# Kernel tuning notes

Hardware: AMD Instinct MI355X
Metric: run time of the kernel (lower is better)

## Reference

```python
import jax, jax.numpy as jnp
import numpy as np

BLOCK_M = 64          # Triton BLOCK_M assumed from first autotune config
SPEAKER, SCENE, STAGE = 1, 2, 3
NUM_HEADS, HEAD_SIZE = 12, 64


def setup_inputs() -> dict:
    key = jax.random.key(0)
    ks = jax.random.split(key, 6)
    B, T, E = 4, 1024, 768
    H, D = NUM_HEADS, HEAD_SIZE
    x = jax.random.normal(ks[0], (B, T, E), jnp.float32)
    idx = jax.random.randint(ks[1], (B, T), 0, 32000)
    struct_embed = jax.random.normal(ks[2], (4, E), jnp.float32) * 0.02
    w_qkv = jax.random.normal(ks[3], (3 * H * D, E), jnp.float32) * 0.02
    w_out = jax.random.normal(ks[4], (E, H * D), jnp.float32) * 0.02
    b_out = jnp.zeros((E,), jnp.float32)
    return {"x": x, "idx": idx, "struct_embed": struct_embed,
            "w_qkv": w_qkv, "w_out": w_out, "b_out": b_out}


def _attention(q, k, v):
    # q,k,v: [B,H,T,D]. Faithful to the Triton kernel (eval mode):
    # q/k rounded to bf16, fp32 dot, logit clamp [-30,30], exp clamp 1e5,
    # +1e-10 denom, output rounded to bf16. Query rows with
    # (row % BLOCK_M) % 3 == 0 are zeroed by the kernel's load mask.
    T, D = q.shape[2], q.shape[3]
    keep = ((jnp.arange(T) % BLOCK_M) % 3 != 0).astype(q.dtype)
    qb = q.astype(jnp.bfloat16).astype(jnp.float32) * keep[None, None, :, None]
    kb = k.astype(jnp.bfloat16).astype(jnp.float32)
    scale = 1.0 / np.sqrt(D).astype(np.float32)
    scores = jnp.einsum('bhmd,bhnd->bhmn', qb, kb) * scale
    scores = jnp.clip(scores, -30.0, 30.0)
    m = jnp.max(scores, axis=-1, keepdims=True)
    p = jnp.minimum(jnp.exp(scores - m), 1e5)
    acc = jnp.einsum('bhmn,bhnd->bhmd', p, v)
    out = acc / (jnp.sum(p, axis=-1, keepdims=True) + 1e-10)
    return out.astype(jnp.bfloat16).astype(jnp.float32)


def reference(x, idx, struct_embed, w_qkv, w_out, b_out):
    B, T, E = x.shape
    H, D = NUM_HEADS, HEAD_SIZE
    # structure embedding addition (struct_dropout is identity in eval)
    struct_ids = ((idx == SPEAKER) * 1 + (idx == SCENE) * 2
                  + (idx == STAGE) * 3)
    x = x + struct_embed[struct_ids]
    # fused QKV projection (no bias)
    qkv = x @ w_qkv.T                              # [B,T,3HD]
    q, k, v = jnp.split(qkv, 3, axis=-1)
    q = q.reshape(B, T, H, D).transpose(0, 2, 1, 3)
    k = k.reshape(B, T, H, D).transpose(0, 2, 1, 3)
    v = v.reshape(B, T, H, D).transpose(0, 2, 1, 3)
    attn = _attention(q, k, v)                     # [B,H,T,D]
    attn = attn.transpose(0, 2, 1, 3).reshape(B, T, H * D)
    return attn @ w_out.T + b_out
```

## Files before the change

### kernel.cpp

```cpp
#include <hip/hip_runtime.h>
#include <hip/hip_bf16.h>

typedef __attribute__((ext_vector_type(8))) short bf16x8;
typedef __attribute__((ext_vector_type(4))) short bf16x4;
typedef __attribute__((ext_vector_type(4))) float f32x4;

#define MFMA16(a, b, c) __builtin_amdgcn_mfma_f32_16x16x32_bf16(a, b, c, 0, 0, 0)

__device__ __forceinline__ unsigned short f2bf(float f) {
  unsigned u = __float_as_uint(f);
  u += 0x7fff + ((u >> 16) & 1);
  return (unsigned short)(u >> 16);
}
__device__ __forceinline__ float bf2f(unsigned short s) {
  return __uint_as_float(((unsigned)s) << 16);
}
__device__ __forceinline__ void gload16(const unsigned short* g, unsigned short* l) {
  __builtin_amdgcn_global_load_lds((const __attribute__((address_space(1))) void*)g,
                                   (__attribute__((address_space(3))) void*)l, 16, 0, 0);
}

__global__ __launch_bounds__(256) void prep_x(const float* __restrict__ x,
                                              const int* __restrict__ idx,
                                              const float* __restrict__ se,
                                              unsigned short* __restrict__ xb) {
  int i = blockIdx.x * 256 + threadIdx.x;
  int row = i / 192, c4 = i % 192;
  int id = idx[row];
  int sid = (id == 1) ? 1 : (id == 2) ? 2 : (id == 3) ? 3 : 0;
  float4 v = ((const float4*)x)[i];
  float4 s = ((const float4*)se)[sid * 192 + c4];
  ushort4 o;
  o.x = f2bf(v.x + s.x); o.y = f2bf(v.y + s.y);
  o.z = f2bf(v.z + s.z); o.w = f2bf(v.w + s.w);
  *(ushort4*)(xb + (size_t)i * 4) = o;
}

__global__ __launch_bounds__(256) void conv_w(const float* __restrict__ w,
                                              unsigned short* __restrict__ o, int n4) {
  int i = blockIdx.x * 256 + threadIdx.x;
  if (i >= n4) return;
  float4 v = ((const float4*)w)[i];
  ushort4 u;
  u.x = f2bf(v.x); u.y = f2bf(v.y); u.z = f2bf(v.z); u.w = f2bf(v.w);
  ((ushort4*)o)[i] = u;
}

template <int MODE>
__global__ __launch_bounds__(256) void gemm_bt(const unsigned short* __restrict__ A,
                                               const unsigned short* __restrict__ B,
                                               void* __restrict__ Cout,
                                               const float* __restrict__ bias,
                                               unsigned short* __restrict__ vT,
                                               int N, int K) {
  __shared__ unsigned short As[128 * 32];
  __shared__ unsigned short Bs[128 * 32];
  int tid = threadIdx.x;
  int lane = tid & 63, wid = tid >> 6;
  int l15 = lane & 15, lhi = lane >> 4;
  int wr = wid >> 1, wc = wid & 1;
  long tm = (long)blockIdx.x * 128;
  long tn = (long)blockIdx.y * 128;
  f32x4 acc[4][4];
  const f32x4 z4 = {0.f, 0.f, 0.f, 0.f};
  for (int i = 0; i < 4; ++i)
    for (int j = 0; j < 4; ++j) acc[i][j] = z4;

  int wbase = tid & ~63;
  for (int k0 = 0; k0 < K; k0 += 32) {
    __syncthreads();
    for (int p = 0; p < 2; ++p) {
      int tt = p * 256 + tid;
      int row = tt >> 2;
      int kc = (tt & 3) * 8;
      gload16(&A[(tm + row) * (long)K + k0 + kc], &As[(size_t)(p * 256 + wbase) * 8]);
      gload16(&B[(tn + row) * (long)K + k0 + kc], &Bs[(size_t)(p * 256 + wbase) * 8]);
    }
    __syncthreads();
    bf16x8 af[4], bfr[4];
#pragma unroll
    for (int mi = 0; mi < 4; ++mi)
      af[mi] = *(const bf16x8*)&As[(wr * 64 + mi * 16 + l15) * 32 + lhi * 8];
#pragma unroll
    for (int nj = 0; nj < 4; ++nj)
      bfr[nj] = *(const bf16x8*)&Bs[(wc * 64 + nj * 16 + l15) * 32 + lhi * 8];
#pragma unroll
    for (int mi = 0; mi < 4; ++mi)
#pragma unroll
      for (int nj = 0; nj < 4; ++nj)
        acc[mi][nj] = MFMA16(af[mi], bfr[nj], acc[mi][nj]);
  }

  bool isV = (MODE == 1) && (tn >= 1536);
  if (isV) {
    int b = (int)(tm >> 10);
    int hbase = (int)((tn - 1536) >> 6) + wc;
    int tb = (int)(tm & 1023) + wr * 64 + lhi * 4;
#pragma unroll
    for (int nj = 0; nj < 4; ++nj) {
      int dd = nj * 16 + l15;
      size_t vbase = ((size_t)(b * 12 + hbase)) * 65536 + (size_t)dd * 1024;
#pragma unroll
      for (int mi = 0; mi < 4; ++mi) {
        ushort4 o;
        o.x = f2bf(acc[mi][nj][0]); o.y = f2bf(acc[mi][nj][1]);
        o.z = f2bf(acc[mi][nj][2]); o.w = f2bf(acc[mi][nj][3]);
        *(ushort4*)&vT[vbase + tb + mi * 16] = o;
      }
    }
    return;
  }

#pragma unroll
  for (int mi = 0; mi < 4; ++mi) {
    long row = tm + wr * 64 + mi * 16 + lhi * 4;
#pragma unroll
    for (int nj = 0; nj < 4; ++nj) {
      long col = tn + wc * 64 + nj * 16 + l15;
      float bv = (MODE == 0) ? bias[col] : 0.f;
#pragma unroll
      for (int r = 0; r < 4; ++r) {
        float v = acc[mi][nj][r];
        if (MODE == 1) {
          ((unsigned short*)Cout)[(row + r) * (long)N + col] = f2bf(v);
        } else {
          ((float*)Cout)[(row + r) * (long)N + col] = v + bv;
        }
      }
    }
  }
}

__global__ __launch_bounds__(256) void attn_fwd(const unsigned short* __restrict__ qkv,
                                                const unsigned short* __restrict__ vT,
                                                unsigned short* __restrict__ attnb) {
  __shared__ unsigned short Ks[2][4096];
  __shared__ unsigned short Vs[2][4096];
  int tid = threadIdx.x;
  int lane = tid & 63, w = tid >> 6;
  int l15 = lane & 15, lhi = lane >> 4;
  int sw = l15 & 7;
  int qt = blockIdx.x, bh = blockIdx.y;
  int b = bh / 12, h = bh % 12;

  int r8 = lane >> 3;
  int cK = ((lane & 7) ^ r8) << 3;
  int wbase = (tid & ~63) * 8;
  const unsigned short* kg = qkv + (size_t)(b * 1024) * 2304 + 768 + h * 64 + cK;
  const unsigned short* vg = vT + (size_t)bh * 65536 + cK;

#pragma unroll
  for (int p = 0; p < 2; ++p) {
    int row = p * 32 + w * 8 + r8;
    gload16(kg + (size_t)row * 2304, &Ks[0][p * 2048 + wbase]);
    gload16(vg + (size_t)row * 1024, &Vs[0][p * 2048 + wbase]);
  }

  int qrow = w * 16 + l15;
  bf16x8 qf0 = {0, 0, 0, 0, 0, 0, 0, 0}, qf1 = {0, 0, 0, 0, 0, 0, 0, 0};
  if (qrow % 3 != 0) {
    const unsigned short* qp =
        &qkv[(size_t)(b * 1024 + qt * 64 + qrow) * 2304 + h * 64 + lhi * 8];
    qf0 = *(const bf16x8*)qp;
    qf1 = *(const bf16x8*)(qp + 32);
  }

  const f32x4 z4 = {0.f, 0.f, 0.f, 0.f};
  f32x4 acc[4];
#pragma unroll
  for (int dg = 0; dg < 4; ++dg) acc[dg] = z4;
  float lsum = 0.f;

  __syncthreads();

  int buf = 0;
  for (int t = 0; t < 16; ++t) {
    if (t < 15) {
      size_t k0 = (size_t)(t + 1) * 64;
#pragma unroll
      for (int p = 0; p < 2; ++p) {
        int row = p * 32 + w * 8 + r8;
        gload16(kg + (k0 + row) * 2304, &Ks[buf ^ 1][p * 2048 + wbase]);
        gload16(vg + (size_t)row * 1024 + k0, &Vs[buf ^ 1][p * 2048 + wbase]);
      }
    }
    const unsigned short* ks = Ks[buf];
    const unsigned short* vs = Vs[buf];
    bf16x8 paf[2];
#pragma unroll
    for (int g = 0; g < 4; ++g) {
      const unsigned short* kr = &ks[(g * 16 + l15) * 64];
      bf16x8 kf0 = *(const bf16x8*)&kr[(lhi ^ sw) << 3];
      bf16x8 kf1 = *(const bf16x8*)&kr[((lhi + 4) ^ sw) << 3];
      f32x4 sg = MFMA16(kf0, qf0, z4);
      sg = MFMA16(kf1, qf1, sg);
#pragma unroll
      for (int r = 0; r < 4; ++r) {
        float pv = __expf(sg[r] * 0.125f);
        unsigned short ub = f2bf(pv);
        lsum += bf2f(ub);
        paf[g >> 1][(g & 1) * 4 + r] = (short)ub;
      }
    }
#pragma unroll
    for (int dg = 0; dg < 4; ++dg) {
      const unsigned short* vr = &vs[(dg * 16 + l15) * 64];
#pragma unroll
      for (int kh = 0; kh < 2; ++kh) {
        int o0 = kh * 32 + lhi * 4;
        int o1 = o0 + 16;
        bf16x4 v0 = *(const bf16x4*)&vr[(((o0 >> 3) ^ sw) << 3) + (o0 & 7)];
        bf16x4 v1 = *(const bf16x4*)&vr[(((o1 >> 3) ^ sw) << 3) + (o1 & 7)];
        bf16x8 vf = __builtin_shufflevector(v0, v1, 0, 1, 2, 3, 4, 5, 6, 7);
        acc[dg] = MFMA16(paf[kh], vf, acc[dg]);
      }
    }
    __syncthreads();
    buf ^= 1;
  }

  float st = lsum;
  st += __shfl_xor(st, 16);
  st += __shfl_xor(st, 32);
#pragma unroll
  for (int r = 0; r < 4; ++r) {
    float den = __shfl(st, lhi * 4 + r);
    float inv = 1.f / (den + 1e-10f);
    int orow = qt * 64 + w * 16 + lhi * 4 + r;
    size_t obase = (size_t)(b * 1024 + orow) * 768 + h * 64;
#pragma unroll
    for (int dg = 0; dg < 4; ++dg)
      attnb[obase + dg * 16 + l15] = f2bf(acc[dg][r] * inv);
  }
}

extern "C" void kernel_launch(void* const* d_in, const int* in_sizes, int n_in,
                              void* d_out, int out_size, void* d_ws, size_t ws_size,
                              hipStream_t stream) {
  (void)in_sizes; (void)n_in; (void)out_size; (void)ws_size;
  const float* x    = (const float*)d_in[0];
  const int*   idx  = (const int*)d_in[1];
  const float* se   = (const float*)d_in[2];
  const float* wqkv = (const float*)d_in[3];
  const float* wout = (const float*)d_in[4];
  const float* bout = (const float*)d_in[5];
  float* out = (float*)d_out;

  char* ws = (char*)d_ws;
  unsigned short* xb    = (unsigned short*)(ws);
  unsigned short* wqkvb = (unsigned short*)(ws + 6291456);
  unsigned short* woutb = (unsigned short*)(ws + 9830400);
  unsigned short* qkvb  = (unsigned short*)(ws + 11010048);
  unsigned short* vT    = (unsigned short*)(ws + 29884416);
  unsigned short* attnb = (unsigned short*)(ws + 36175872);

  prep_x<<<3072, 256, 0, stream>>>(x, idx, se, xb);
  conv_w<<<1728, 256, 0, stream>>>(wqkv, wqkvb, 442368);
  conv_w<<<576, 256, 0, stream>>>(wout, woutb, 147456);
  gemm_bt<1><<<dim3(32, 18), 256, 0, stream>>>(xb, wqkvb, qkvb, nullptr, vT, 2304, 768);
  attn_fwd<<<dim3(16, 48), 256, 0, stream>>>(qkvb, vT, attnb);
  gemm_bt<0><<<dim3(32, 6), 256, 0, stream>>>(attnb, woutb, out, bout, nullptr, 768, 768);
}
```

Baseline: 94.97 us.

## Double attention query tile per block and fuse prep kernels into one launch

The attention kernel now handles 128 query rows per block, two 16-row sub-tiles per wave, so each K/V tile loaded into LDS feeds twice as many MFMAs and the grid shrinks to 8x48 blocks. It also raises wave priority around the PV MFMA section. The three input-conversion kernels are merged into a single launch to save launch overhead. The cost is more registers per wave and fewer blocks, which may reduce occupancy on a large GPU.

```diff
diff --git a/kernel.cpp b/kernel.cpp
--- a/kernel.cpp
+++ b/kernel.cpp
@@ -20,30 +20,40 @@
                                    (__attribute__((address_space(3))) void*)l, 16, 0, 0);
 }
 
-__global__ __launch_bounds__(256) void prep_x(const float* __restrict__ x,
-                                              const int* __restrict__ idx,
-                                              const float* __restrict__ se,
-                                              unsigned short* __restrict__ xb) {
-  int i = blockIdx.x * 256 + threadIdx.x;
-  int row = i / 192, c4 = i % 192;
-  int id = idx[row];
-  int sid = (id == 1) ? 1 : (id == 2) ? 2 : (id == 3) ? 3 : 0;
-  float4 v = ((const float4*)x)[i];
-  float4 s = ((const float4*)se)[sid * 192 + c4];
-  ushort4 o;
-  o.x = f2bf(v.x + s.x); o.y = f2bf(v.y + s.y);
-  o.z = f2bf(v.z + s.z); o.w = f2bf(v.w + s.w);
-  *(ushort4*)(xb + (size_t)i * 4) = o;
-}
-
-__global__ __launch_bounds__(256) void conv_w(const float* __restrict__ w,
-                                              unsigned short* __restrict__ o, int n4) {
-  int i = blockIdx.x * 256 + threadIdx.x;
-  if (i >= n4) return;
-  float4 v = ((const float4*)w)[i];
-  ushort4 u;
-  u.x = f2bf(v.x); u.y = f2bf(v.y); u.z = f2bf(v.z); u.w = f2bf(v.w);
-  ((ushort4*)o)[i] = u;
+__global__ __launch_bounds__(256) void prep_all(const float* __restrict__ x,
+                                                const int* __restrict__ idx,
+                                                const float* __restrict__ se,
+                                                const float* __restrict__ wqkv,
+                                                const float* __restrict__ wout,
+                                                unsigned short* __restrict__ xb,
+                                                unsigned short* __restrict__ wqkvb,
+                                                unsigned short* __restrict__ woutb) {
+  int bid = blockIdx.x;
+  int tid = threadIdx.x;
+  if (bid < 3072) {
+    int i = bid * 256 + tid;
+    int row = i / 192, c4 = i % 192;
+    int id = idx[row];
+    int sid = (id == 1) ? 1 : (id == 2) ? 2 : (id == 3) ? 3 : 0;
+    float4 v = ((const float4*)x)[i];
+    float4 s = ((const float4*)se)[sid * 192 + c4];
+    ushort4 o;
+    o.x = f2bf(v.x + s.x); o.y = f2bf(v.y + s.y);
+    o.z = f2bf(v.z + s.z); o.w = f2bf(v.w + s.w);
+    *(ushort4*)(xb + (size_t)i * 4) = o;
+  } else if (bid < 3072 + 1728) {
+    int i = (bid - 3072) * 256 + tid;
+    float4 v = ((const float4*)wqkv)[i];
+    ushort4 u;
+    u.x = f2bf(v.x); u.y = f2bf(v.y); u.z = f2bf(v.z); u.w = f2bf(v.w);
+    ((ushort4*)wqkvb)[i] = u;
+  } else {
+    int i = (bid - 4800) * 256 + tid;
+    float4 v = ((const float4*)wout)[i];
+    ushort4 u;
+    u.x = f2bf(v.x); u.y = f2bf(v.y); u.z = f2bf(v.z); u.w = f2bf(v.w);
+    ((ushort4*)woutb)[i] = u;
+  }
 }
 
 template <int MODE>
@@ -156,20 +166,27 @@
     gload16(vg + (size_t)row * 1024, &Vs[0][p * 2048 + wbase]);
   }
 
-  int qrow = w * 16 + l15;
-  bf16x8 qf0 = {0, 0, 0, 0, 0, 0, 0, 0}, qf1 = {0, 0, 0, 0, 0, 0, 0, 0};
-  if (qrow % 3 != 0) {
-    const unsigned short* qp =
-        &qkv[(size_t)(b * 1024 + qt * 64 + qrow) * 2304 + h * 64 + lhi * 8];
-    qf0 = *(const bf16x8*)qp;
-    qf1 = *(const bf16x8*)(qp + 32);
+  bf16x8 qf[2][2];
+#pragma unroll
+  for (int u = 0; u < 2; ++u) {
+    qf[u][0] = bf16x8{0, 0, 0, 0, 0, 0, 0, 0};
+    qf[u][1] = bf16x8{0, 0, 0, 0, 0, 0, 0, 0};
+    int lrow = ((w * 32 + u * 16) & 63) + l15;
+    if (lrow % 3 != 0) {
+      const unsigned short* qp =
+          &qkv[(size_t)(b * 1024 + qt * 128 + w * 32 + u * 16 + l15) * 2304 + h * 64 + lhi * 8];
+      qf[u][0] = *(const bf16x8*)qp;
+      qf[u][1] = *(const bf16x8*)(qp + 32);
+    }
   }
 
   const f32x4 z4 = {0.f, 0.f, 0.f, 0.f};
-  f32x4 acc[4];
-#pragma unroll
-  for (int dg = 0; dg < 4; ++dg) acc[dg] = z4;
-  float lsum = 0.f;
+  f32x4 acc[2][4];
+#pragma unroll
+  for (int u = 0; u < 2; ++u)
+#pragma unroll
+    for (int dg = 0; dg < 4; ++dg) acc[u][dg] = z4;
+  float lsum[2] = {0.f, 0.f};
 
   __syncthreads();
 
@@ -186,22 +203,28 @@
     }
     const unsigned short* ks = Ks[buf];
     const unsigned short* vs = Vs[buf];
-    bf16x8 paf[2];
+
+    bf16x8 paf[2][2];
 #pragma unroll
     for (int g = 0; g < 4; ++g) {
       const unsigned short* kr = &ks[(g * 16 + l15) * 64];
       bf16x8 kf0 = *(const bf16x8*)&kr[(lhi ^ sw) << 3];
       bf16x8 kf1 = *(const bf16x8*)&kr[((lhi + 4) ^ sw) << 3];
-      f32x4 sg = MFMA16(kf0, qf0, z4);
-      sg = MFMA16(kf1, qf1, sg);
-#pragma unroll
-      for (int r = 0; r < 4; ++r) {
-        float pv = __expf(sg[r] * 0.125f);
-        unsigned short ub = f2bf(pv);
-        lsum += bf2f(ub);
-        paf[g >> 1][(g & 1) * 4 + r] = (short)ub;
-      }
-    }
+#pragma unroll
+      for (int u = 0; u < 2; ++u) {
+        f32x4 sg = MFMA16(kf0, qf[u][0], z4);
+        sg = MFMA16(kf1, qf[u][1], sg);
+#pragma unroll
+        for (int r = 0; r < 4; ++r) {
+          float pv = __expf(sg[r] * 0.125f);
+          unsigned short ub = f2bf(pv);
+          lsum[u] += bf2f(ub);
+          paf[u][g >> 1][(g & 1) * 4 + r] = (short)ub;
+        }
+      }
+    }
+
+    __builtin_amdgcn_s_setprio(1);
 #pragma unroll
     for (int dg = 0; dg < 4; ++dg) {
       const unsigned short* vr = &vs[(dg * 16 + l15) * 64];
@@ -212,25 +235,31 @@
         bf16x4 v0 = *(const bf16x4*)&vr[(((o0 >> 3) ^ sw) << 3) + (o0 & 7)];
         bf16x4 v1 = *(const bf16x4*)&vr[(((o1 >> 3) ^ sw) << 3) + (o1 & 7)];
         bf16x8 vf = __builtin_shufflevector(v0, v1, 0, 1, 2, 3, 4, 5, 6, 7);
-        acc[dg] = MFMA16(paf[kh], vf, acc[dg]);
-      }
-    }
+#pragma unroll
+        for (int u = 0; u < 2; ++u)
+          acc[u][dg] = MFMA16(paf[u][kh], vf, acc[u][dg]);
+      }
+    }
+    __builtin_amdgcn_s_setprio(0);
     __syncthreads();
     buf ^= 1;
   }
 
-  float st = lsum;
-  st += __shfl_xor(st, 16);
-  st += __shfl_xor(st, 32);
-#pragma unroll
-  for (int r = 0; r < 4; ++r) {
-    float den = __shfl(st, lhi * 4 + r);
-    float inv = 1.f / (den + 1e-10f);
-    int orow = qt * 64 + w * 16 + lhi * 4 + r;
-    size_t obase = (size_t)(b * 1024 + orow) * 768 + h * 64;
-#pragma unroll
-    for (int dg = 0; dg < 4; ++dg)
-      attnb[obase + dg * 16 + l15] = f2bf(acc[dg][r] * inv);
+#pragma unroll
+  for (int u = 0; u < 2; ++u) {
+    float st = lsum[u];
+    st += __shfl_xor(st, 16);
+    st += __shfl_xor(st, 32);
+#pragma unroll
+    for (int r = 0; r < 4; ++r) {
+      float den = __shfl(st, lhi * 4 + r);
+      float inv = 1.f / (den + 1e-10f);
+      int orow = qt * 128 + w * 32 + u * 16 + lhi * 4 + r;
+      size_t obase = (size_t)(b * 1024 + orow) * 768 + h * 64;
+#pragma unroll
+      for (int dg = 0; dg < 4; ++dg)
+        attnb[obase + dg * 16 + l15] = f2bf(acc[u][dg][r] * inv);
+    }
   }
 }
 
@@ -254,10 +283,8 @@
   unsigned short* vT    = (unsigned short*)(ws + 29884416);
   unsigned short* attnb = (unsigned short*)(ws + 36175872);
 
-  prep_x<<<3072, 256, 0, stream>>>(x, idx, se, xb);
-  conv_w<<<1728, 256, 0, stream>>>(wqkv, wqkvb, 442368);
-  conv_w<<<576, 256, 0, stream>>>(wout, woutb, 147456);
+  prep_all<<<5376, 256, 0, stream>>>(x, idx, se, wqkv, wout, xb, wqkvb, woutb);
   gemm_bt<1><<<dim3(32, 18), 256, 0, stream>>>(xb, wqkvb, qkvb, nullptr, vT, 2304, 768);
-  attn_fwd<<<dim3(16, 48), 256, 0, stream>>>(qkvb, vT, attnb);
+  attn_fwd<<<dim3(8, 48), 256, 0, stream>>>(qkvb, vT, attnb);
   gemm_bt<0><<<dim3(32, 6), 256, 0, stream>>>(attnb, woutb, out, bout, nullptr, 768, 768);
 }
```

After: 95.34 us. Within noise of the previous version (+0.4%).
